# Performance work log

Hardware: AMD Instinct MI355X
Metric: run time of the kernel (lower is better)

Reference implementation:

```python
import jax, jax.numpy as jnp
import numpy as np


def lstm_step(x_t, h, c, Wih, Whh, bih, bhh):
    # PyTorch LSTM gate order: i, f, g, o
    gates = x_t @ Wih.T + h @ Whh.T + bih + bhh
    i, f, g, o = jnp.split(gates, 4, axis=-1)
    i = jax.nn.sigmoid(i)
    f = jax.nn.sigmoid(f)
    g = jnp.tanh(g)
    o = jax.nn.sigmoid(o)
    c_new = f * c + i * g
    h_new = o * jnp.tanh(c_new)
    return h_new, c_new


def setup_inputs() -> dict:
    key = jax.random.key(0)
    N, C, T, V, M = 512, 3, 300, 25, 2
    F = C * V * M  # 150
    H = 100
    ks = jax.random.split(key, 12)
    s = 1.0 / np.sqrt(H)  # PyTorch LSTM/Linear init scale
    u = lambda k, shape: jax.random.uniform(k, shape, jnp.float32, -s, s)
    return {
        "x": jax.random.normal(ks[0], (N, C, T, V, M), jnp.float32),
        "enc_Wih": u(ks[1], (4 * H, F)),
        "enc_Whh": u(ks[2], (4 * H, H)),
        "enc_bih": u(ks[3], (4 * H,)),
        "enc_bhh": u(ks[4], (4 * H,)),
        "dec_Wih": u(ks[5], (4 * H, F)),
        "dec_Whh": u(ks[6], (4 * H, H)),
        "dec_bih": u(ks[7], (4 * H,)),
        "dec_bhh": u(ks[8], (4 * H,)),
        "fc_W": u(ks[9], (F, H)),
        "fc_b": u(ks[10], (F,)),
    }


def reference(x, enc_Wih, enc_Whh, enc_bih, enc_bhh,
              dec_Wih, dec_Whh, dec_bih, dec_bhh, fc_W, fc_b):
    N, C, T, V, M = x.shape
    F = C * V * M
    H = enc_Whh.shape[1]
    # (N,C,T,V,M) -> (N,T,C*V*M)
    xs = jnp.transpose(x, (0, 2, 1, 3, 4)).reshape(N, T, F)

    # Encoder LSTM: only need final (h, c)
    h0 = jnp.zeros((N, H), x.dtype)
    c0 = jnp.zeros((N, H), x.dtype)

    def enc_step(carry, xt):
        h, c = carry
        h, c = lstm_step(xt, h, c, enc_Wih, enc_Whh, enc_bih, enc_bhh)
        return (h, c), None

    (h, c), _ = jax.lax.scan(enc_step, (h0, c0), jnp.swapaxes(xs, 0, 1))

    inp0 = jnp.zeros((N, F), x.dtype)

    def dec_step(carry, _):
        inp, h, c = carry
        h, c = lstm_step(inp, h, c, dec_Wih, dec_Whh, dec_bih, dec_bhh)
        out = h @ fc_W.T + fc_b
        return (out, h, c), out

    _, outs = jax.lax.scan(dec_step, (inp0, h, c), None, length=T - 1)  # [T-1,N,F]

    # outputs[:,0,:] stays zero, like the torch.zeros buffer
    outputs = jnp.concatenate([jnp.zeros((1, N, F), x.dtype), outs], axis=0)  # [T,N,F]
    outputs = jnp.swapaxes(outputs, 0, 1).reshape(N, T, C, V, M)
    return jnp.transpose(outputs, (0, 2, 1, 3, 4))  # (N,C,T,V,M)
```

## Files before the change

kernel.cpp:

```cpp
#include <hip/hip_runtime.h>
#include <hip/hip_fp16.h>


#define B_HIST   0u
#define HIST_STRIDE 29952
#define B_W2S    30670848u
#define B_BEFFS  30830848u
#define B_AWIH   30832448u
#define B_AENC   30975808u
#define B_ADEC1  31090496u
#define B_ADEC2  31205184u
#define B_BENCF  31319872u
#define B_B1F    31348544u
#define B_BEFFF  31377216u
#define B_AFCW   31405888u
#define B_XG     31446848u
#define XG_PER_BG 4300800u

typedef _Float16 f16x8 __attribute__((ext_vector_type(8)));
typedef float    f32x4 __attribute__((ext_vector_type(4)));

#define WG_BARRIER() asm volatile("s_waitcnt lgkmcnt(0)\n\ts_barrier" ::: "memory")

__device__ __forceinline__ unsigned pkrtz(float a, float b) {
  return __builtin_bit_cast(unsigned, __builtin_amdgcn_cvt_pkrtz(a, b));
}
__device__ __forceinline__ unsigned pack2f(float a, float b) {
  return (unsigned)__half_as_ushort(__float2half(a)) |
         ((unsigned)__half_as_ushort(__float2half(b)) << 16);
}
__device__ __forceinline__ float fast_sig(float x) {
  float e = __builtin_amdgcn_exp2f(x * -1.442695040888963f);
  return __builtin_amdgcn_rcpf(1.f + e);
}
__device__ __forceinline__ float fast_tanh(float x) {
  float e = __builtin_amdgcn_exp2f(x * -2.885390081777926f);
  return fmaf(2.f, __builtin_amdgcn_rcpf(1.f + e), -1.f);
}
__device__ __forceinline__ f32x4 mfma16(uint4 a, uint4 b, f32x4 c) {
  return __builtin_amdgcn_mfma_f32_16x16x32_f16(
      __builtin_bit_cast(f16x8, a), __builtin_bit_cast(f16x8, b), c, 0, 0, 0);
}
__device__ __forceinline__ float uslo(unsigned u) {
  return __half2float(__ushort_as_half((unsigned short)(u & 0xffffu)));
}
__device__ __forceinline__ float ushi(unsigned u) {
  return __half2float(__ushort_as_half((unsigned short)(u >> 16)));
}

__global__ void prep_w2(const float* __restrict__ dWih, const float* __restrict__ dWhh,
                        const float* __restrict__ dbih, const float* __restrict__ dbhh,
                        const float* __restrict__ fcW,  const float* __restrict__ fcb,
                        char* __restrict__ wsb)
{
  int idx = blockIdx.x * 256 + threadIdx.x;
  if (idx < 40000) {
    int r = idx / 100, j = idx - r * 100;
    float s = 0.f;
    for (int f = 0; f < 150; ++f) s = fmaf(dWih[r * 150 + f], fcW[f * 100 + j], s);
    ((float*)(wsb + B_W2S))[idx] = dWhh[r * 100 + j] + s;
  } else if (idx < 40400) {
    int r = idx - 40000;
    float s = 0.f;
    for (int f = 0; f < 150; ++f) s = fmaf(dWih[r * 150 + f], fcb[f], s);
    ((float*)(wsb + B_BEFFS))[r] = dbih[r] + dbhh[r] + s;
  }
}

__global__ void prep_frags(const float* __restrict__ eWih, const float* __restrict__ eWhh,
                           const float* __restrict__ dWhh, const float* __restrict__ fcW,
                           const float* __restrict__ ebih, const float* __restrict__ ebhh,
                           const float* __restrict__ dbih, const float* __restrict__ dbhh,
                           char* __restrict__ wsb)
{
  int idx = blockIdx.x * 256 + threadIdx.x;
  const float* w2s = (const float*)(wsb + B_W2S);
  const float* beffs = (const float*)(wsb + B_BEFFS);
  if (idx < 8960) {
    int l = idx & 63, fi = idx >> 6;
    int kc = fi % 5, mt = fi / 5;
    int w = mt >> 2, ty = mt & 3;
    int gr = w * 16 + (l & 15);
    int r = ty * 100 + gr;
    int k0 = kc * 32 + (l >> 4) * 8;
    unsigned u[4];
    for (int p = 0; p < 4; ++p) {
      int k = k0 + 2 * p;
      float v0 = (gr < 100 && k     < 150) ? eWih[r * 150 + k]     : 0.f;
      float v1 = (gr < 100 && k + 1 < 150) ? eWih[r * 150 + k + 1] : 0.f;
      u[p] = pack2f(v0, v1);
    }
    ((uint4*)(wsb + B_AWIH))[idx] = make_uint4(u[0], u[1], u[2], u[3]);
  } else if (idx < 8960 + 3 * 7168) {
    int t = idx - 8960;
    int set = t / 7168, q = t - set * 7168;
    int l = q & 63, fi = q >> 6;
    int kc = fi & 3, mt = fi >> 2;
    int w = mt >> 2, ty = mt & 3;
    int gr = w * 16 + (l & 15);
    int r = ty * 100 + gr;
    int k0 = kc * 32 + (l >> 4) * 8;
    unsigned u[4];
    for (int p = 0; p < 4; ++p) {
      int k = k0 + 2 * p;
      float v0 = 0.f, v1 = 0.f;
      if (gr < 100) {
        if (k < 100)     v0 = set == 0 ? eWhh[r*100+k]   : set == 1 ? dWhh[r*100+k]   : w2s[r*100+k];
        if (k + 1 < 100) v1 = set == 0 ? eWhh[r*100+k+1] : set == 1 ? dWhh[r*100+k+1] : w2s[r*100+k+1];
      }
      u[p] = pack2f(v0, v1);
    }
    ((uint4*)(wsb + B_AENC + (unsigned)set * 114688u))[q] = make_uint4(u[0], u[1], u[2], u[3]);
  } else if (idx < 8960 + 21504 + 3 * 1792) {
    int t = idx - 8960 - 21504;
    int set = t / 1792, q = t - set * 1792;
    int l = q & 63, mt = q >> 6;
    int w = mt >> 2, ty = mt & 3;
    float v[4];
    for (int rr = 0; rr < 4; ++rr) {
      int gr = w * 16 + (l >> 4) * 4 + rr;
      int r = ty * 100 + gr;
      v[rr] = 0.f;
      if (gr < 100)
        v[rr] = set == 0 ? ebih[r] + ebhh[r] : set == 1 ? dbih[r] + dbhh[r] : beffs[r];
    }
    ((float4*)(wsb + B_BENCF + (unsigned)set * 28672u))[q] = make_float4(v[0], v[1], v[2], v[3]);
  } else if (idx < 35840 + 2560) {
    int q2 = idx - 35840;
    int l = q2 & 63, fi = q2 >> 6;
    int kc = fi & 3, mt = fi >> 2;
    int f = mt * 16 + (l & 15);
    int k0 = kc * 32 + (l >> 4) * 8;
    unsigned u[4];
    for (int p = 0; p < 4; ++p) {
      int k = k0 + 2 * p;
      float v0 = (f < 150 && k     < 100) ? fcW[f * 100 + k]     : 0.f;
      float v1 = (f < 150 && k + 1 < 100) ? fcW[f * 100 + k + 1] : 0.f;
      u[p] = pack2f(v0, v1);
    }
    ((uint4*)(wsb + B_AFCW))[q2] = make_uint4(u[0], u[1], u[2], u[3]);
  }
}

__global__ __launch_bounds__(64)
void pre(const float* __restrict__ x, char* __restrict__ wsb, int nbase)
{
  const int l = threadIdx.x;
  const int tg = blockIdx.x;
  const int b  = blockIdx.y;
  const int quad = l >> 4, nn = l & 15;
  __shared__ unsigned short xls[4][16][168];

  const int t0 = tg * 4;
  const int n0 = nbase + b * 16;
  for (int it = 0; it < 84; ++it) {
    int i = l + it * 64;
    int tp = i / 1344; int rem = i - tp * 1344;
    int np = rem / 84; int p = rem - np * 84;
    unsigned val = 0;
    if (p < 75) {
      int c = p * 2 / 50; int q = p * 2 - c * 50;
      const float2 v = *(const float2*)(x + (size_t)(n0 + np) * 45000 + c * 15000 + (t0 + tp) * 50 + q);
      val = pkrtz(v.x, v.y);
    }
    *(unsigned*)&xls[tp][np][2 * p] = val;
  }
  __syncthreads();

  uint4 B[4][5];
#pragma unroll
  for (int u = 0; u < 4; ++u)
#pragma unroll
    for (int kc = 0; kc < 5; ++kc)
      B[u][kc] = *(const uint4*)&xls[u][nn][kc * 32 + quad * 8];

  const uint4* awih = (const uint4*)(wsb + B_AWIH);
  const float4* bencf = (const float4*)(wsb + B_BENCF);
  unsigned short* xgo = (unsigned short*)(wsb + B_XG);

  for (int w = 0; w < 7; ++w) {
    unsigned st[4][8];
#pragma unroll
    for (int ty = 0; ty < 4; ++ty) {
      const int mt = w * 4 + ty;
      uint4 A0 = awih[(mt * 5 + 0) * 64 + l];
      uint4 A1 = awih[(mt * 5 + 1) * 64 + l];
      uint4 A2 = awih[(mt * 5 + 2) * 64 + l];
      uint4 A3 = awih[(mt * 5 + 3) * 64 + l];
      uint4 A4 = awih[(mt * 5 + 4) * 64 + l];
      float4 bi = bencf[mt * 64 + l];
      f32x4 bias; bias[0] = bi.x; bias[1] = bi.y; bias[2] = bi.z; bias[3] = bi.w;
#pragma unroll
      for (int u = 0; u < 4; ++u) {
        f32x4 acc = bias;
        acc = mfma16(A0, B[u][0], acc);
        acc = mfma16(A1, B[u][1], acc);
        acc = mfma16(A2, B[u][2], acc);
        acc = mfma16(A3, B[u][3], acc);
        acc = mfma16(A4, B[u][4], acc);
        st[u][ty * 2 + 0] = pkrtz(acc[0], acc[1]);
        st[u][ty * 2 + 1] = pkrtz(acc[2], acc[3]);
      }
    }
#pragma unroll
    for (int u = 0; u < 4; ++u) {
      size_t off = ((size_t)(b * 300 + t0 + u) * 7 + w) * 1024 + (size_t)l * 16;
      *(uint4*)(xgo + off)     = make_uint4(st[u][0], st[u][1], st[u][2], st[u][3]);
      *(uint4*)(xgo + off + 8) = make_uint4(st[u][4], st[u][5], st[u][6], st[u][7]);
    }
  }
}

__global__ __launch_bounds__(448)
void recurrent(char* __restrict__ wsb, int nbase)
{
  const int tid = threadIdx.x;
  const int l = tid & 63, w = tid >> 6;
  const int quad = l >> 4, n = l & 15;
  const int c0 = w * 16 + quad * 4;
  __shared__ unsigned short hbuf[2][16][136];

  for (int i = tid; i < 2176; i += 448) ((unsigned*)hbuf)[i] = 0;

  const uint4* aenc  = (const uint4*)(wsb + B_AENC);
  const uint4* adec1 = (const uint4*)(wsb + B_ADEC1);
  const uint4* adec2 = (const uint4*)(wsb + B_ADEC2);
  uint4 A[4][4];
#pragma unroll
  for (int ty = 0; ty < 4; ++ty)
#pragma unroll
    for (int kc = 0; kc < 4; ++kc)
      A[ty][kc] = aenc[((w * 4 + ty) * 4 + kc) * 64 + l];

  f32x4 bias[4];
  float cst[4] = {0.f, 0.f, 0.f, 0.f};

  const uint4* xgw = (const uint4*)(wsb + B_XG) + (size_t)blockIdx.x * 300 * 896 + (w * 64 + l) * 2;
  uint4 pxa[2], pxb[2];
  pxa[0] = xgw[0];   pxb[0] = xgw[1];
  pxa[1] = xgw[896]; pxb[1] = xgw[897];

  unsigned short* hist = (unsigned short*)(wsb + B_HIST) +
                         (size_t)(nbase + blockIdx.x * 16 + n) * HIST_STRIDE + c0;
  const bool hist_on = (c0 < 100);

  for (int g = 0; g < 599; ++g) {
    WG_BARRIER();
    const int rd = g & 1, wr = rd ^ 1;
    uint4 B0 = *(const uint4*)&hbuf[rd][n][0  + quad * 8];
    uint4 B1 = *(const uint4*)&hbuf[rd][n][32 + quad * 8];
    uint4 B2 = *(const uint4*)&hbuf[rd][n][64 + quad * 8];
    uint4 B3 = *(const uint4*)&hbuf[rd][n][96 + quad * 8];

    f32x4 acc[4];
    if (g < 300) {
      const int sl = g & 1;
      uint4 xa = pxa[sl], xb = pxb[sl];
      acc[0][0] = uslo(xa.x); acc[0][1] = ushi(xa.x); acc[0][2] = uslo(xa.y); acc[0][3] = ushi(xa.y);
      acc[1][0] = uslo(xa.z); acc[1][1] = ushi(xa.z); acc[1][2] = uslo(xa.w); acc[1][3] = ushi(xa.w);
      acc[2][0] = uslo(xb.x); acc[2][1] = ushi(xb.x); acc[2][2] = uslo(xb.y); acc[2][3] = ushi(xb.y);
      acc[3][0] = uslo(xb.z); acc[3][1] = ushi(xb.z); acc[3][2] = uslo(xb.w); acc[3][3] = ushi(xb.w);
      if (g + 2 < 300) { const uint4* p = xgw + (size_t)(g + 2) * 896; pxa[sl] = p[0]; pxb[sl] = p[1]; }
    } else {
#pragma unroll
      for (int ty = 0; ty < 4; ++ty) acc[ty] = bias[ty];
    }

#pragma unroll
    for (int kc = 0; kc < 4; ++kc) {
      uint4 Bk = (kc == 0) ? B0 : (kc == 1) ? B1 : (kc == 2) ? B2 : B3;
#pragma unroll
      for (int ty = 0; ty < 4; ++ty) acc[ty] = mfma16(A[ty][kc], Bk, acc[ty]);
    }

    float hv[4];
#pragma unroll
    for (int r = 0; r < 4; ++r) {
      float si = fast_sig(acc[0][r]);
      float sf = fast_sig(acc[1][r]);
      float tg = fast_tanh(acc[2][r]);
      float so = fast_sig(acc[3][r]);
      cst[r] = fmaf(sf, cst[r], si * tg);
      hv[r] = so * fast_tanh(cst[r]);
    }
    unsigned u0 = pkrtz(hv[0], hv[1]);
    unsigned u1 = pkrtz(hv[2], hv[3]);
    *(uint2*)&hbuf[wr][n][c0] = make_uint2(u0, u1);
    if (g >= 300 && hist_on)
      *(uint2*)(hist + (size_t)(g - 300) * 100) = make_uint2(u0, u1);

    if (g == 299) {
#pragma unroll
      for (int ty = 0; ty < 4; ++ty) {
#pragma unroll
        for (int kc = 0; kc < 4; ++kc) A[ty][kc] = adec1[((w * 4 + ty) * 4 + kc) * 64 + l];
        float4 bv = ((const float4*)(wsb + B_B1F))[(w * 4 + ty) * 64 + l];
        bias[ty][0] = bv.x; bias[ty][1] = bv.y; bias[ty][2] = bv.z; bias[ty][3] = bv.w;
      }
    } else if (g == 300) {
#pragma unroll
      for (int ty = 0; ty < 4; ++ty) {
#pragma unroll
        for (int kc = 0; kc < 4; ++kc) A[ty][kc] = adec2[((w * 4 + ty) * 4 + kc) * 64 + l];
        float4 bv = ((const float4*)(wsb + B_BEFFF))[(w * 4 + ty) * 64 + l];
        bias[ty][0] = bv.x; bias[ty][1] = bv.y; bias[ty][2] = bv.z; bias[ty][3] = bv.w;
      }
    }
  }
}

__global__ __launch_bounds__(64)
void emit(const char* __restrict__ wsb, const float* __restrict__ fcb, float* __restrict__ out)
{
  const int l = threadIdx.x;
  const int n = blockIdx.x;
  const int quad = l >> 4, col = l & 15;
  const uint4* afcw = (const uint4*)(wsb + B_AFCW);
  const unsigned short* hist_n = (const unsigned short*)(wsb + B_HIST) + (size_t)n * HIST_STRIDE;
  float* on_ = out + (size_t)n * 45000;

  for (int i = l; i < 150; i += 64) on_[(i / 50) * 15000 + (i % 50)] = 0.f;

  uint4 A[10][4];
#pragma unroll
  for (int mt = 0; mt < 10; ++mt)
#pragma unroll
    for (int kc = 0; kc < 4; ++kc)
      A[mt][kc] = afcw[(mt * 4 + kc) * 64 + l];

  float fcbv[10][4];
#pragma unroll
  for (int mt = 0; mt < 10; ++mt)
#pragma unroll
    for (int r = 0; r < 4; ++r) {
      int f = mt * 16 + quad * 4 + r;
      fcbv[mt][r] = (f < 150) ? fcb[f] : 0.f;
    }

  for (int tt = 0; tt < 19; ++tt) {
    const int t0 = 1 + tt * 16;
    const int th = t0 + col - 1;
    const unsigned short* hb = hist_n + (size_t)th * 100 + quad * 8;
    uint4 B0 = *(const uint4*)(hb);
    uint4 B1 = *(const uint4*)(hb + 32);
    uint4 B2 = *(const uint4*)(hb + 64);
    uint4 B3 = *(const uint4*)(hb + 96);
    const int t = t0 + col;
    const bool ton = (t <= 299);
#pragma unroll
    for (int mt = 0; mt < 10; ++mt) {
      f32x4 acc;
      acc[0] = fcbv[mt][0]; acc[1] = fcbv[mt][1]; acc[2] = fcbv[mt][2]; acc[3] = fcbv[mt][3];
      acc = mfma16(A[mt][0], B0, acc);
      acc = mfma16(A[mt][1], B1, acc);
      acc = mfma16(A[mt][2], B2, acc);
      acc = mfma16(A[mt][3], B3, acc);
#pragma unroll
      for (int r = 0; r < 4; ++r) {
        const int f = mt * 16 + quad * 4 + r;
        if (ton && f < 150) {
          const int c = f / 50, vm = f - c * 50;
          on_[c * 15000 + t * 50 + vm] = acc[r];
        }
      }
    }
  }
}

extern "C" void kernel_launch(void* const* d_in, const int* in_sizes, int n_in,
                              void* d_out, int out_size, void* d_ws, size_t ws_size,
                              hipStream_t stream) {
  const float* x    = (const float*)d_in[0];
  const float* eWih = (const float*)d_in[1];
  const float* eWhh = (const float*)d_in[2];
  const float* ebih = (const float*)d_in[3];
  const float* ebhh = (const float*)d_in[4];
  const float* dWih = (const float*)d_in[5];
  const float* dWhh = (const float*)d_in[6];
  const float* dbih = (const float*)d_in[7];
  const float* dbhh = (const float*)d_in[8];
  const float* fcW  = (const float*)d_in[9];
  const float* fcb  = (const float*)d_in[10];
  float* out = (float*)d_out;
  char* wsb  = (char*)d_ws;

  int npass = 1;
  while (npass < 32) {
    if ((size_t)B_XG + (size_t)(32 / npass) * XG_PER_BG <= ws_size) break;
    npass *= 2;
  }
  const int bg = 32 / npass;

  prep_w2<<<158, 256, 0, stream>>>(dWih, dWhh, dbih, dbhh, fcW, fcb, wsb);
  prep_frags<<<150, 256, 0, stream>>>(eWih, eWhh, dWhh, fcW, ebih, ebhh, dbih, dbhh, wsb);
  for (int p = 0; p < npass; ++p) {
    pre<<<dim3(75, bg), 64, 0, stream>>>(x, wsb, p * bg * 16);
    recurrent<<<bg, 448, 0, stream>>>(wsb, p * bg * 16);
  }
  emit<<<512, 64, 0, stream>>>(wsb, fcb, out);
}
```

Before: 1.189 ms.

## Batch gate reciprocals with Montgomery trick and request two workgroups per CU

Replaces the per-element rcp in sigmoid/tanh with a batched reciprocal: products of eight denominators, one rcp, then back-substitution. Exponent arguments are clamped to ±15 so the products stay in float range. This trades transcendental-unit ops for extra multiplies on the serial recurrence critical path. It also sets launch_bounds(448,2) and shrinks x-gate prefetch from two steps ahead to one, cutting registers to fit two workgroups per CU at the cost of less load-latency hiding. The clamping and product chain add small numerical error.

```diff
diff --git a/kernel.cpp b/kernel.cpp
--- a/kernel.cpp
+++ b/kernel.cpp
@@ -22,6 +22,10 @@
 
 #define WG_BARRIER() asm volatile("s_waitcnt lgkmcnt(0)\n\ts_barrier" ::: "memory")
 
+#define L1X 1.442695040888963f
+#define L2X 2.885390081777926f
+#define ACLAMP 15.0f
+
 __device__ __forceinline__ unsigned pkrtz(float a, float b) {
   return __builtin_bit_cast(unsigned, __builtin_amdgcn_cvt_pkrtz(a, b));
 }
@@ -29,14 +33,6 @@
   return (unsigned)__half_as_ushort(__float2half(a)) |
          ((unsigned)__half_as_ushort(__float2half(b)) << 16);
 }
-__device__ __forceinline__ float fast_sig(float x) {
-  float e = __builtin_amdgcn_exp2f(x * -1.442695040888963f);
-  return __builtin_amdgcn_rcpf(1.f + e);
-}
-__device__ __forceinline__ float fast_tanh(float x) {
-  float e = __builtin_amdgcn_exp2f(x * -2.885390081777926f);
-  return fmaf(2.f, __builtin_amdgcn_rcpf(1.f + e), -1.f);
-}
 __device__ __forceinline__ f32x4 mfma16(uint4 a, uint4 b, f32x4 c) {
   return __builtin_amdgcn_mfma_f32_16x16x32_f16(
       __builtin_bit_cast(f16x8, a), __builtin_bit_cast(f16x8, b), c, 0, 0, 0);
@@ -46,6 +42,35 @@
 }
 __device__ __forceinline__ float ushi(unsigned u) {
   return __half2float(__ushort_as_half((unsigned short)(u >> 16)));
+}
+__device__ __forceinline__ float clampe(float x) {
+  return fminf(fmaxf(x, -ACLAMP), ACLAMP);
+}
+__device__ __forceinline__ float mkden(float acc, float k) {
+  return 1.f + __builtin_amdgcn_exp2f(clampe(acc * k));
+}
+__device__ __forceinline__ void recip8(const float* d, float* o) {
+  float p1 = d[0] * d[1], p2 = p1 * d[2], p3 = p2 * d[3];
+  float p4 = p3 * d[4], p5 = p4 * d[5], p6 = p5 * d[6], p7 = p6 * d[7];
+  float s = __builtin_amdgcn_rcpf(p7);
+  o[7] = s * p6; s *= d[7];
+  o[6] = s * p5; s *= d[6];
+  o[5] = s * p4; s *= d[5];
+  o[4] = s * p3; s *= d[4];
+  o[3] = s * p2; s *= d[3];
+  o[2] = s * p1; s *= d[2];
+  o[1] = s * d[0]; o[0] = s * d[1];
+}
+__device__ __forceinline__ void recip4(const float* d, float* o) {
+  float p1 = d[0] * d[1], p2 = p1 * d[2], p3 = p2 * d[3];
+  float s = __builtin_amdgcn_rcpf(p3);
+  o[3] = s * p2; s *= d[3];
+  o[2] = s * p1; s *= d[2];
+  o[1] = s * d[0]; o[0] = s * d[1];
+}
+typedef _Float16 h2_t __attribute__((ext_vector_type(2)));
+__device__ __forceinline__ float fdot2u(unsigned a, unsigned b, float c) {
+  return __builtin_amdgcn_fdot2(__builtin_bit_cast(h2_t, a), __builtin_bit_cast(h2_t, b), c, false);
 }
 
 __global__ void prep_w2(const float* __restrict__ dWih, const float* __restrict__ dWhh,
@@ -211,7 +236,7 @@
   }
 }
 
-__global__ __launch_bounds__(448)
+__global__ __launch_bounds__(448, 2)
 void recurrent(char* __restrict__ wsb, int nbase)
 {
   const int tid = threadIdx.x;
@@ -236,9 +261,7 @@
   float cst[4] = {0.f, 0.f, 0.f, 0.f};
 
   const uint4* xgw = (const uint4*)(wsb + B_XG) + (size_t)blockIdx.x * 300 * 896 + (w * 64 + l) * 2;
-  uint4 pxa[2], pxb[2];
-  pxa[0] = xgw[0];   pxb[0] = xgw[1];
-  pxa[1] = xgw[896]; pxb[1] = xgw[897];
+  uint4 xa = xgw[0], xb = xgw[1];
 
   unsigned short* hist = (unsigned short*)(wsb + B_HIST) +
                          (size_t)(nbase + blockIdx.x * 16 + n) * HIST_STRIDE + c0;
@@ -254,13 +277,11 @@
 
     f32x4 acc[4];
     if (g < 300) {
-      const int sl = g & 1;
-      uint4 xa = pxa[sl], xb = pxb[sl];
       acc[0][0] = uslo(xa.x); acc[0][1] = ushi(xa.x); acc[0][2] = uslo(xa.y); acc[0][3] = ushi(xa.y);
       acc[1][0] = uslo(xa.z); acc[1][1] = ushi(xa.z); acc[1][2] = uslo(xa.w); acc[1][3] = ushi(xa.w);
       acc[2][0] = uslo(xb.x); acc[2][1] = ushi(xb.x); acc[2][2] = uslo(xb.y); acc[2][3] = ushi(xb.y);
       acc[3][0] = uslo(xb.z); acc[3][1] = ushi(xb.z); acc[3][2] = uslo(xb.w); acc[3][3] = ushi(xb.w);
-      if (g + 2 < 300) { const uint4* p = xgw + (size_t)(g + 2) * 896; pxa[sl] = p[0]; pxb[sl] = p[1]; }
+      if (g + 1 < 300) { const uint4* p = xgw + (size_t)(g + 1) * 896; xa = p[0]; xb = p[1]; }
     } else {
 #pragma unroll
       for (int ty = 0; ty < 4; ++ty) acc[ty] = bias[ty];
@@ -273,16 +294,32 @@
       for (int ty = 0; ty < 4; ++ty) acc[ty] = mfma16(A[ty][kc], Bk, acc[ty]);
     }
 
+    float den[16], sg[16];
+#pragma unroll
+    for (int ty = 0; ty < 4; ++ty) {
+      const float k = (ty == 2) ? -L2X : -L1X;
+#pragma unroll
+      for (int r = 0; r < 4; ++r) den[ty * 4 + r] = mkden(acc[ty][r], k);
+    }
+    recip8(den + 0, sg + 0);
+    recip8(den + 8, sg + 8);
+
+    float so[4];
+#pragma unroll
+    for (int r = 0; r < 4; ++r) {
+      float si = sg[0 + r], sf = sg[4 + r];
+      float tg = fmaf(2.f, sg[8 + r], -1.f);
+      so[r] = sg[12 + r];
+      cst[r] = fmaf(sf, cst[r], si * tg);
+    }
+    float dc[4], rc[4];
+#pragma unroll
+    for (int r = 0; r < 4; ++r) dc[r] = mkden(cst[r], -L2X);
+    recip4(dc, rc);
     float hv[4];
 #pragma unroll
-    for (int r = 0; r < 4; ++r) {
-      float si = fast_sig(acc[0][r]);
-      float sf = fast_sig(acc[1][r]);
-      float tg = fast_tanh(acc[2][r]);
-      float so = fast_sig(acc[3][r]);
-      cst[r] = fmaf(sf, cst[r], si * tg);
-      hv[r] = so * fast_tanh(cst[r]);
-    }
+    for (int r = 0; r < 4; ++r) hv[r] = so[r] * fmaf(2.f, rc[r], -1.f);
+
     unsigned u0 = pkrtz(hv[0], hv[1]);
     unsigned u1 = pkrtz(hv[2], hv[3]);
     *(uint2*)&hbuf[wr][n][c0] = make_uint2(u0, u1);
```

Result: slower. 1.217 ms (+2.4%).
